# Kernel optimization log

Measured on AMD Instinct MI355X. Metric: run time of the kernel, lower is better.

The kernel has to match this reference:

```python
import jax, jax.numpy as jnp
import numpy as np

N_ENT = 100000
N_USR = 1024
E = 400000
D = 128
H = 4
R = 32


def setup_inputs() -> dict:
    key = jax.random.key(0)
    ks = jax.random.split(key, 9)
    a = float(np.sqrt(6.0 / (D + D)))  # xavier_uniform bound for [D, D]
    return {
        "entity_emb": jax.random.normal(ks[0], (N_ENT, D), dtype=jnp.float32),
        "user_emb": jax.random.normal(ks[1], (N_USR, D), dtype=jnp.float32),
        "interact_mat": jnp.zeros((1,), dtype=jnp.float32),  # unused by forward
        "weight": jax.random.normal(ks[2], (R, D), dtype=jnp.float32) * 0.1,
        "qTrans": jax.random.uniform(ks[3], (D, D), minval=-a, maxval=a, dtype=jnp.float32),
        "kTrans": jax.random.uniform(ks[4], (D, D), minval=-a, maxval=a, dtype=jnp.float32),
        "vTrans": jax.random.uniform(ks[5], (D, D), minval=-a, maxval=a, dtype=jnp.float32),
        "edge_index": jax.random.randint(ks[6], (2, E), 0, N_ENT, dtype=jnp.int64)
            if jax.config.jax_enable_x64 else jax.random.randint(ks[6], (2, E), 0, N_ENT, dtype=jnp.int32),
        "edge_type": jax.random.randint(ks[7], (E,), 1, R + 1, dtype=jnp.int32),  # types in [1, R]
        "layer": 0,
    }


def _kglayer(rows, col_embeds, embeds, n_seg, qT, kT, vT):
    # rows: [E] target-node index, col_embeds: [E, D] edge messages
    dh = D // H
    row_embeds = embeds[rows]                              # gather [E, D]
    q = (row_embeds @ qT).reshape(-1, H, dh)
    k = (col_embeds @ kT).reshape(-1, H, dh)
    v = (col_embeds @ vT).reshape(-1, H, dh)
    att = jnp.clip(jnp.einsum("ehd,ehd->eh", q, k), -10.0, 10.0)
    exp_att = jnp.exp(att)                                 # [E, H]
    att_norm = jax.ops.segment_sum(exp_att, rows, num_segments=n_seg)[rows]
    att = exp_att / (att_norm + 1e-8)
    res = (att[..., None] * v).reshape(-1, D)              # [E, D]
    return jax.ops.segment_sum(res, rows, num_segments=n_seg)


def _sim_hrt(head_emb, tail_emb, rel_emb):
    # per-edge scalar attention logit [E, 1]
    tr = jnp.linalg.norm(tail_emb * rel_emb, axis=1, keepdims=True)
    hr = jnp.linalg.norm(head_emb * rel_emb, axis=1, keepdims=True)
    return (hr * tr) ** 2


def reference(entity_emb, user_emb, interact_mat, weight, qTrans, kTrans, vTrans,
              edge_index, edge_type, layer):
    n_entities = entity_emb.shape[0]
    head, tail = edge_index[0], edge_index[1]
    rel = weight[edge_type - 1]                            # [E, D]
    neigh = entity_emb[tail] * rel                         # [E, D]
    kg_emb = _kglayer(head, neigh, entity_emb, n_entities, qTrans, kTrans, vTrans)
    w = _sim_hrt(kg_emb[head], kg_emb[tail], rel)          # [E, 1]
    w = jnp.broadcast_to(w, neigh.shape)                   # expand to [E, D]
    # scatter_softmax over edges sharing the same head (numerically stable)
    m = jax.ops.segment_max(w, head, num_segments=n_entities)[head]
    e = jnp.exp(w - m)
    s = jax.ops.segment_sum(e, head, num_segments=n_entities)[head]
    soft = e / s
    msg = soft * entity_emb[tail]
    return jax.ops.segment_sum(msg, head, num_segments=n_entities)
```

## Files before the change

kernel.cpp:

```cpp
#include <hip/hip_runtime.h>
#include <cstdint>

#define D 128
#define H 4
#define N_ENT 100000
#define N_EDGE 400000
#define R 32

#define SCAN_NB ((N_ENT + 511) / 512)

__global__ void k_hist(const int* __restrict__ head, int* __restrict__ deg) {
  const int e = blockIdx.x * 256 + threadIdx.x;
  if (e < N_EDGE) atomicAdd(&deg[head[e]], 1);
}

__global__ __launch_bounds__(256) void k_scan1(const int* __restrict__ deg,
                                               int* __restrict__ bsum) {
  const int t = threadIdx.x;
  const int i = blockIdx.x * 512 + t * 2;
  int v0 = (i < N_ENT) ? deg[i] : 0;
  int v1 = (i + 1 < N_ENT) ? deg[i + 1] : 0;
  int s = v0 + v1;
#pragma unroll
  for (int k = 1; k < 64; k <<= 1) s += __shfl_xor(s, k);
  __shared__ int ws[4];
  if ((t & 63) == 0) ws[t >> 6] = s;
  __syncthreads();
  if (t == 0) bsum[blockIdx.x] = ws[0] + ws[1] + ws[2] + ws[3];
}

__global__ __launch_bounds__(256) void k_scan2(const int* __restrict__ bsum,
                                               int* __restrict__ bbase,
                                               int* __restrict__ off) {
  __shared__ int sh[256];
  const int t = threadIdx.x;
  const int v = (t < SCAN_NB) ? bsum[t] : 0;
  sh[t] = v;
  __syncthreads();
  for (int d = 1; d < 256; d <<= 1) {
    const int u = (t >= d) ? sh[t - d] : 0;
    __syncthreads();
    sh[t] += u;
    __syncthreads();
  }
  if (t < SCAN_NB) bbase[t] = sh[t] - v;
  if (t == SCAN_NB - 1) off[N_ENT] = sh[t];
}

__global__ __launch_bounds__(256) void k_scan3(const int* __restrict__ deg,
                                               const int* __restrict__ bbase,
                                               int* __restrict__ off,
                                               int* __restrict__ cur) {
  __shared__ int sh[256];
  const int t = threadIdx.x;
  const int i = blockIdx.x * 512 + t * 2;
  const int v0 = (i < N_ENT) ? deg[i] : 0;
  const int v1 = (i + 1 < N_ENT) ? deg[i + 1] : 0;
  const int s = v0 + v1;
  sh[t] = s;
  __syncthreads();
  for (int d = 1; d < 256; d <<= 1) {
    const int u = (t >= d) ? sh[t - d] : 0;
    __syncthreads();
    sh[t] += u;
    __syncthreads();
  }
  const int ex = sh[t] - s + bbase[blockIdx.x];
  if (i < N_ENT) {
    off[i] = ex;
    cur[i] = ex;
  }
  if (i + 1 < N_ENT) {
    off[i + 1] = ex + v0;
    cur[i + 1] = ex + v0;
  }
}

__global__ void k_scatter(const int* __restrict__ head,
                          const int* __restrict__ tail,
                          const int* __restrict__ etype, int* __restrict__ cur,
                          int2* __restrict__ teP) {
  const int e = blockIdx.x * 256 + threadIdx.x;
  if (e >= N_EDGE) return;
  const int hd = head[e];
  const int pos = atomicAdd(&cur[hd], 1);
  teP[pos] = make_int2(tail[e], etype[e] - 1);
}

__global__ __launch_bounds__(256) void k_tr(const float* __restrict__ in,
                                            float* __restrict__ out) {
  __shared__ float tile[32][33];
  const int bx = blockIdx.x & 3, by = blockIdx.x >> 2;
  const int c = threadIdx.x & 31;
  const int r0 = (threadIdx.x >> 5) * 4;
#pragma unroll
  for (int i = 0; i < 4; ++i)
    tile[r0 + i][c] = in[(by * 32 + r0 + i) * 128 + bx * 32 + c];
  __syncthreads();
#pragma unroll
  for (int i = 0; i < 4; ++i)
    out[(bx * 32 + r0 + i) * 128 + by * 32 + c] = tile[c][r0 + i];
}

__global__ __launch_bounds__(512) void k_qproj(const float* __restrict__ ent,
                                               const float* __restrict__ qT,
                                               float* __restrict__ Q) {
  __shared__ float sT[D * D];
  __shared__ float rows[D * 128];
  const int t = threadIdx.x;
  const int n0 = blockIdx.x * 128;
#pragma unroll
  for (int s = 0; s < 8; ++s) {
    const int idx = (s * 512 + t) * 4;
    *(float4*)&sT[idx] = *(const float4*)&qT[idx];
  }
  {
    const int g = t & 3;
    const int n = t >> 2;
    const int node = n0 + n;
    if (node < N_ENT) {
      const float* src = ent + (size_t)node * D;
#pragma unroll
      for (int s = 0; s < 8; ++s) {
        const int i = s * 16 + g * 4;
        float4 v = *(const float4*)&src[i];
        rows[(i + 0) * 128 + n] = v.x;
        rows[(i + 1) * 128 + n] = v.y;
        rows[(i + 2) * 128 + n] = v.z;
        rows[(i + 3) * 128 + n] = v.w;
      }
    } else {
#pragma unroll
      for (int s = 0; s < 8; ++s) {
        const int i = s * 16 + g * 4;
        rows[(i + 0) * 128 + n] = 0.f;
        rows[(i + 1) * 128 + n] = 0.f;
        rows[(i + 2) * 128 + n] = 0.f;
        rows[(i + 3) * 128 + n] = 0.f;
      }
    }
  }
  __syncthreads();
  const int jj = t & 15;
  const int ee = t >> 4;
  float acc[4][8];
#pragma unroll
  for (int a = 0; a < 4; ++a)
#pragma unroll
    for (int b = 0; b < 8; ++b) acc[a][b] = 0.f;
#pragma unroll 4
  for (int i = 0; i < D; ++i) {
    float4 b0 = *(float4*)&sT[i * D + jj * 8];
    float4 b1 = *(float4*)&sT[i * D + jj * 8 + 4];
    float4 a0 = *(float4*)&rows[i * 128 + ee * 4];
    float bv[8] = {b0.x, b0.y, b0.z, b0.w, b1.x, b1.y, b1.z, b1.w};
    float av[4] = {a0.x, a0.y, a0.z, a0.w};
#pragma unroll
    for (int a = 0; a < 4; ++a)
#pragma unroll
      for (int b = 0; b < 8; ++b) acc[a][b] = fmaf(av[a], bv[b], acc[a][b]);
  }
#pragma unroll
  for (int a = 0; a < 4; ++a) {
    const int node = n0 + ee * 4 + a;
    if (node < N_ENT) {
      float4 o0 = {acc[a][0], acc[a][1], acc[a][2], acc[a][3]};
      float4 o1 = {acc[a][4], acc[a][5], acc[a][6], acc[a][7]};
      *(float4*)&Q[(size_t)node * D + jj * 8] = o0;
      *(float4*)&Q[(size_t)node * D + jj * 8 + 4] = o1;
    }
  }
}

__global__ __launch_bounds__(256, 8) void k_fused(
    const float* __restrict__ ent, const float* __restrict__ wrel,
    const float* __restrict__ kTt, const float* __restrict__ vT, float* qkg,
    const int* __restrict__ off, const int2* __restrict__ teP) {
  __shared__ float sQ[8 * 128];
  __shared__ float sPA[8 * 512];
  const int t = threadIdx.x;
  const int base = blockIdx.x * 8;

  const int wid = t >> 6;
  const int half = (t >> 5) & 1;
  const int l32 = t & 31;
  const int kk = wid * 2 + half;
  const int n = base + kk;

  {
    const int k = t >> 5;
    const int c4 = (t & 31) * 4;
    *(float4*)&sQ[k * 128 + c4] =
        *(const float4*)&qkg[(size_t)(base + k) * D + c4];
  }

  const int eb = off[n];
  const int deg = off[n + 1] - eb;
  float4 xv = {0, 0, 0, 0}, rv = {0, 0, 0, 0};
  if (deg > 0) {
    const int2 pf = teP[eb];
    xv = *(const float4*)&ent[(size_t)pf.x * D + l32 * 4];
    rv = *(const float4*)&wrel[(size_t)pf.y * D + l32 * 4];
  }
  __syncthreads();

  {
    const int i = t & 127;
    const int sub = t >> 7;
    float pp[2][8];
#pragma unroll
    for (int hh = 0; hh < 2; ++hh)
#pragma unroll
      for (int k = 0; k < 8; ++k) pp[hh][k] = 0.f;
#pragma unroll
    for (int hh = 0; hh < 2; ++hh) {
      const int h = sub * 2 + hh;
#pragma unroll 2
      for (int c4 = 0; c4 < 8; ++c4) {
        const float kv0 = kTt[(h * 32 + c4 * 4 + 0) * 128 + i];
        const float kv1 = kTt[(h * 32 + c4 * 4 + 1) * 128 + i];
        const float kv2 = kTt[(h * 32 + c4 * 4 + 2) * 128 + i];
        const float kv3 = kTt[(h * 32 + c4 * 4 + 3) * 128 + i];
#pragma unroll
        for (int k = 0; k < 8; ++k) {
          const float4 q = *(const float4*)&sQ[k * 128 + h * 32 + c4 * 4];
          pp[hh][k] = fmaf(kv0, q.x, pp[hh][k]);
          pp[hh][k] = fmaf(kv1, q.y, pp[hh][k]);
          pp[hh][k] = fmaf(kv2, q.z, pp[hh][k]);
          pp[hh][k] = fmaf(kv3, q.w, pp[hh][k]);
        }
      }
    }
#pragma unroll
    for (int hh = 0; hh < 2; ++hh)
#pragma unroll
      for (int k = 0; k < 8; ++k)
        sPA[k * 512 + (sub * 2 + hh) * 128 + i] = pp[hh][k];
  }
  __syncthreads();

  {
    const int lp = l32 & 3;
    const float4 P0 = *(const float4*)&sPA[kk * 512 + 0 * 128 + l32 * 4];
    const float4 P1 = *(const float4*)&sPA[kk * 512 + 1 * 128 + l32 * 4];
    const float4 P2 = *(const float4*)&sPA[kk * 512 + 2 * 128 + l32 * 4];
    const float4 P3 = *(const float4*)&sPA[kk * 512 + 3 * 128 + l32 * 4];
    float4 b0 = {0, 0, 0, 0}, b1 = {0, 0, 0, 0};
    float4 b2 = {0, 0, 0, 0}, b3 = {0, 0, 0, 0};
    float s0 = 0.f, s1 = 0.f, s2 = 0.f, s3 = 0.f;
    for (int idx = 0; idx < deg; ++idx) {
      const float4 cx = xv, cr = rv;
      if (idx + 1 < deg) {
        const int2 pf = teP[eb + idx + 1];
        xv = *(const float4*)&ent[(size_t)pf.x * D + l32 * 4];
        rv = *(const float4*)&wrel[(size_t)pf.y * D + l32 * 4];
      }
      const float4 nh = {cx.x * cr.x, cx.y * cr.y, cx.z * cr.z, cx.w * cr.w};
      float d0 = nh.x * P0.x + nh.y * P0.y + nh.z * P0.z + nh.w * P0.w;
      float d1 = nh.x * P1.x + nh.y * P1.y + nh.z * P1.z + nh.w * P1.w;
      float d2 = nh.x * P2.x + nh.y * P2.y + nh.z * P2.z + nh.w * P2.w;
      float d3 = nh.x * P3.x + nh.y * P3.y + nh.z * P3.z + nh.w * P3.w;
      float x01 = (l32 & 1) ? d1 : d0;
      float y01 = (l32 & 1) ? d0 : d1;
      x01 += __shfl_xor(y01, 1);
      float x23 = (l32 & 1) ? d3 : d2;
      float y23 = (l32 & 1) ? d2 : d3;
      x23 += __shfl_xor(y23, 1);
      float xa = (l32 & 2) ? x23 : x01;
      float xb = (l32 & 2) ? x01 : x23;
      xa += __shfl_xor(xb, 2);
      xa += __shfl_xor(xa, 4);
      xa += __shfl_xor(xa, 8);
      xa += __shfl_xor(xa, 16);
      const float eL = __expf(fminf(fmaxf(xa, -10.f), 10.f));
      const float e0 = eL;
      const float e1 = __shfl_xor(eL, 1);
      const float e2 = __shfl_xor(eL, 2);
      const float e3 = __shfl_xor(eL, 3);
      b0.x = fmaf(e0, nh.x, b0.x); b0.y = fmaf(e0, nh.y, b0.y);
      b0.z = fmaf(e0, nh.z, b0.z); b0.w = fmaf(e0, nh.w, b0.w);
      b1.x = fmaf(e1, nh.x, b1.x); b1.y = fmaf(e1, nh.y, b1.y);
      b1.z = fmaf(e1, nh.z, b1.z); b1.w = fmaf(e1, nh.w, b1.w);
      b2.x = fmaf(e2, nh.x, b2.x); b2.y = fmaf(e2, nh.y, b2.y);
      b2.z = fmaf(e2, nh.z, b2.z); b2.w = fmaf(e2, nh.w, b2.w);
      b3.x = fmaf(e3, nh.x, b3.x); b3.y = fmaf(e3, nh.y, b3.y);
      b3.z = fmaf(e3, nh.z, b3.z); b3.w = fmaf(e3, nh.w, b3.w);
      s0 += e0; s1 += e1; s2 += e2; s3 += e3;
    }
    const float i0 = 1.f / (s0 + 1e-8f);
    const float i1 = 1.f / (s1 + 1e-8f);
    const float i2 = 1.f / (s2 + 1e-8f);
    const float i3 = 1.f / (s3 + 1e-8f);
    float4 o0 = {b0.x * i0, b0.y * i0, b0.z * i0, b0.w * i0};
    float4 o1 = {b1.x * i1, b1.y * i1, b1.z * i1, b1.w * i1};
    float4 o2 = {b2.x * i2, b2.y * i2, b2.z * i2, b2.w * i2};
    float4 o3 = {b3.x * i3, b3.y * i3, b3.z * i3, b3.w * i3};
    const int sb = kk * 512 + l32 * 4;
    *(float4*)&sPA[sb + ((lp ^ 0) << 7)] = o0;
    *(float4*)&sPA[sb + ((lp ^ 1) << 7)] = o1;
    *(float4*)&sPA[sb + ((lp ^ 2) << 7)] = o2;
    *(float4*)&sPA[sb + ((lp ^ 3) << 7)] = o3;
  }
  __syncthreads();

  {
    const int c = t & 127;
    const int g4 = (t >> 7) * 4;
    const int h = c >> 5;
    float acc0 = 0.f, acc1 = 0.f, acc2 = 0.f, acc3 = 0.f;
    const float* agg0 = &sPA[(g4 + 0) * 512 + h * 128];
    const float* agg1 = &sPA[(g4 + 1) * 512 + h * 128];
    const float* agg2 = &sPA[(g4 + 2) * 512 + h * 128];
    const float* agg3 = &sPA[(g4 + 3) * 512 + h * 128];
#pragma unroll 4
    for (int d4 = 0; d4 < 32; ++d4) {
      const float4 a0 = *(const float4*)&agg0[d4 * 4];
      const float4 a1 = *(const float4*)&agg1[d4 * 4];
      const float4 a2 = *(const float4*)&agg2[d4 * 4];
      const float4 a3 = *(const float4*)&agg3[d4 * 4];
      const float v0 = vT[(d4 * 4 + 0) * 128 + c];
      const float v1 = vT[(d4 * 4 + 1) * 128 + c];
      const float v2 = vT[(d4 * 4 + 2) * 128 + c];
      const float v3 = vT[(d4 * 4 + 3) * 128 + c];
      acc0 = fmaf(a0.x, v0, acc0); acc0 = fmaf(a0.y, v1, acc0);
      acc0 = fmaf(a0.z, v2, acc0); acc0 = fmaf(a0.w, v3, acc0);
      acc1 = fmaf(a1.x, v0, acc1); acc1 = fmaf(a1.y, v1, acc1);
      acc1 = fmaf(a1.z, v2, acc1); acc1 = fmaf(a1.w, v3, acc1);
      acc2 = fmaf(a2.x, v0, acc2); acc2 = fmaf(a2.y, v1, acc2);
      acc2 = fmaf(a2.z, v2, acc2); acc2 = fmaf(a2.w, v3, acc2);
      acc3 = fmaf(a3.x, v0, acc3); acc3 = fmaf(a3.y, v1, acc3);
      acc3 = fmaf(a3.z, v2, acc3); acc3 = fmaf(a3.w, v3, acc3);
    }
    qkg[(size_t)(base + g4 + 0) * D + c] = acc0;
    qkg[(size_t)(base + g4 + 1) * D + c] = acc1;
    qkg[(size_t)(base + g4 + 2) * D + c] = acc2;
    qkg[(size_t)(base + g4 + 3) * D + c] = acc3;
  }
}

__global__ __launch_bounds__(256) void k_S(const float* __restrict__ kg,
                                           const float* __restrict__ wrel,
                                           float* __restrict__ S) {
  __shared__ float sB[D * 32];
  __shared__ float sA[D * 64];
  const int t = threadIdx.x;
  const int n0 = blockIdx.x * 64;
  {
    const int r = t & 31;
    const int qg = t >> 5;
#pragma unroll
    for (int s = 0; s < 4; ++s) {
      const int d = qg * 16 + s * 4;
      float4 b = *(const float4*)&wrel[(size_t)r * D + d];
      sB[(d + 0) * 32 + r] = b.x * b.x;
      sB[(d + 1) * 32 + r] = b.y * b.y;
      sB[(d + 2) * 32 + r] = b.z * b.z;
      sB[(d + 3) * 32 + r] = b.w * b.w;
    }
  }
  {
    const int nn = t & 63;
    const int dg = t >> 6;
    const int node = n0 + nn;
#pragma unroll
    for (int s = 0; s < 8; ++s) {
      const int d = dg * 32 + s * 4;
      float4 a = {0, 0, 0, 0};
      if (node < N_ENT) a = *(const float4*)&kg[(size_t)node * D + d];
      sA[(d + 0) * 64 + nn] = a.x * a.x;
      sA[(d + 1) * 64 + nn] = a.y * a.y;
      sA[(d + 2) * 64 + nn] = a.z * a.z;
      sA[(d + 3) * 64 + nn] = a.w * a.w;
    }
  }
  __syncthreads();
  const int nn2 = t >> 2;
  const int rg = t & 3;
  float acc[8];
#pragma unroll
  for (int c = 0; c < 8; ++c) acc[c] = 0.f;
#pragma unroll 4
  for (int d = 0; d < D; ++d) {
    const float a = sA[d * 64 + nn2];
    float4 b0 = *(float4*)&sB[d * 32 + rg * 8];
    float4 b1 = *(float4*)&sB[d * 32 + rg * 8 + 4];
    acc[0] = fmaf(a, b0.x, acc[0]);
    acc[1] = fmaf(a, b0.y, acc[1]);
    acc[2] = fmaf(a, b0.z, acc[2]);
    acc[3] = fmaf(a, b0.w, acc[3]);
    acc[4] = fmaf(a, b1.x, acc[4]);
    acc[5] = fmaf(a, b1.y, acc[5]);
    acc[6] = fmaf(a, b1.z, acc[6]);
    acc[7] = fmaf(a, b1.w, acc[7]);
  }
  const int node = n0 + nn2;
  if (node < N_ENT) {
    float4 o0 = {acc[0], acc[1], acc[2], acc[3]};
    float4 o1 = {acc[4], acc[5], acc[6], acc[7]};
    *(float4*)&S[(size_t)node * 32 + rg * 8] = o0;
    *(float4*)&S[(size_t)node * 32 + rg * 8 + 4] = o1;
  }
}

__global__ __launch_bounds__(256) void k_out2(
    const float* __restrict__ ent, const float* __restrict__ S,
    const int* __restrict__ off, const int2* __restrict__ teP,
    float* __restrict__ out) {
  const int t = threadIdx.x;
  const int wid = t >> 6;
  const int half = (t >> 5) & 1;
  const int l32 = t & 31;
  const int kk = wid * 2 + half;
  const int n = blockIdx.x * 8 + kk;
  if (n >= N_ENT) return;
  const int eb = off[n];
  const int deg = off[n + 1] - eb;
  const float sn = S[(size_t)n * 32 + l32];
  float4 acc = {0, 0, 0, 0};
  float m = 0.f, ssum = 0.f;
  for (int b = 0; b < deg; b += 32) {
    const int idx = b + l32;
    const bool val = idx < deg;
    const int e = eb + (val ? idx : 0);
    const int2 tp = teP[e];
    const int tl = tp.x;
    const int ty = tp.y;
    const float snv = __shfl(sn, ty, 32);
    float w = val ? snv * S[(size_t)tl * 32 + ty] : -1.f;
    float cm = w;
#pragma unroll
    for (int k = 1; k < 32; k <<= 1) cm = fmaxf(cm, __shfl_xor(cm, k));
    const float mnew = fmaxf(m, cm);
    const float scale = __expf(m - mnew);
    const float el = val ? __expf(w - mnew) : 0.f;
    float cs = el;
#pragma unroll
    for (int k = 1; k < 32; k <<= 1) cs += __shfl_xor(cs, k);
    ssum = ssum * scale + cs;
    acc.x *= scale; acc.y *= scale; acc.z *= scale; acc.w *= scale;
    const int cnt = (deg - b < 32) ? deg - b : 32;
    for (int j0 = 0; j0 < cnt; j0 += 4) {
      const int rem = cnt - j0;
      const int t0 = __shfl(tl, j0 + 0, 32);
      float4 r0 = *(const float4*)&ent[(size_t)t0 * D + l32 * 4];
      float4 r1, r2, r3;
      if (rem > 1) {
        const int t1 = __shfl(tl, j0 + 1, 32);
        r1 = *(const float4*)&ent[(size_t)t1 * D + l32 * 4];
      }
      if (rem > 2) {
        const int t2 = __shfl(tl, j0 + 2, 32);
        r2 = *(const float4*)&ent[(size_t)t2 * D + l32 * 4];
      }
      if (rem > 3) {
        const int t3 = __shfl(tl, j0 + 3, 32);
        r3 = *(const float4*)&ent[(size_t)t3 * D + l32 * 4];
      }
      const float w0 = __shfl(el, j0 + 0, 32);
      acc.x = fmaf(w0, r0.x, acc.x); acc.y = fmaf(w0, r0.y, acc.y);
      acc.z = fmaf(w0, r0.z, acc.z); acc.w = fmaf(w0, r0.w, acc.w);
      if (rem > 1) {
        const float w1 = __shfl(el, j0 + 1, 32);
        acc.x = fmaf(w1, r1.x, acc.x); acc.y = fmaf(w1, r1.y, acc.y);
        acc.z = fmaf(w1, r1.z, acc.z); acc.w = fmaf(w1, r1.w, acc.w);
      }
      if (rem > 2) {
        const float w2 = __shfl(el, j0 + 2, 32);
        acc.x = fmaf(w2, r2.x, acc.x); acc.y = fmaf(w2, r2.y, acc.y);
        acc.z = fmaf(w2, r2.z, acc.z); acc.w = fmaf(w2, r2.w, acc.w);
      }
      if (rem > 3) {
        const float w3 = __shfl(el, j0 + 3, 32);
        acc.x = fmaf(w3, r3.x, acc.x); acc.y = fmaf(w3, r3.y, acc.y);
        acc.z = fmaf(w3, r3.z, acc.z); acc.w = fmaf(w3, r3.w, acc.w);
      }
    }
    m = mnew;
  }
  const float inv = (deg > 0) ? 1.f / ssum : 0.f;
  float4 o = {acc.x * inv, acc.y * inv, acc.z * inv, acc.w * inv};
  *(float4*)&out[(size_t)n * D + l32 * 4] = o;
}

extern "C" void kernel_launch(void* const* d_in, const int* in_sizes, int n_in,
                              void* d_out, int out_size, void* d_ws,
                              size_t ws_size, hipStream_t stream) {
  const float* ent = (const float*)d_in[0];
  const float* wrel = (const float*)d_in[3];
  const float* qT = (const float*)d_in[4];
  const float* kT = (const float*)d_in[5];
  const float* vT = (const float*)d_in[6];
  const int* eidx = (const int*)d_in[7];
  const int* etype = (const int*)d_in[8];
  const int* head = eidx;
  const int* tail = eidx + N_EDGE;

  float* S = (float*)d_ws;
  int* off = (int*)(S + (size_t)N_ENT * 32);
  int* cur = off + (N_ENT + 2);
  int* deg = cur + N_ENT;
  int* bsum = deg + N_ENT;
  int* bbase = bsum + SCAN_NB;
  int2* teP = (int2*)(bbase + SCAN_NB);
  float* kTt = (float*)(teP + N_EDGE);
  float* qkg = (float*)d_out;

  hipMemsetAsync(deg, 0, N_ENT * sizeof(int), stream);
  k_hist<<<(N_EDGE + 255) / 256, 256, 0, stream>>>(head, deg);
  k_scan1<<<SCAN_NB, 256, 0, stream>>>(deg, bsum);
  k_scan2<<<1, 256, 0, stream>>>(bsum, bbase, off);
  k_scan3<<<SCAN_NB, 256, 0, stream>>>(deg, bbase, off, cur);
  k_scatter<<<(N_EDGE + 255) / 256, 256, 0, stream>>>(head, tail, etype, cur,
                                                      teP);
  k_tr<<<16, 256, 0, stream>>>(kT, kTt);
  k_qproj<<<(N_ENT + 127) / 128, 512, 0, stream>>>(ent, qT, qkg);
  k_fused<<<N_ENT / 8, 256, 0, stream>>>(ent, wrel, kTt, vT, qkg, off, teP);
  k_S<<<(N_ENT + 63) / 64, 256, 0, stream>>>(qkg, wrel, S);
  k_out2<<<(N_ENT + 7) / 8, 256, 0, stream>>>(ent, S, off, teP, qkg);
}
```

Measured before the change: 504.1 us.

## Sort nodes by degree via counting-sort permutation for load-balanced node processing

Adds a degree histogram, scan and scatter that build a permutation of nodes grouped by in-degree (capped at 63). The fused attention kernel and the output kernel then process nodes in that order, so nodes sharing a block or wavefront have similar edge counts and lanes diverge less. The cost is three extra small kernels plus a memset, one indirection per node, and scattered rather than contiguous row reads and writes of qkg. Buffers already used for the scan (cur, bsum, bbase) are reused for the permutation and bins.

```diff
diff --git a/kernel.cpp b/kernel.cpp
--- a/kernel.cpp
+++ b/kernel.cpp
@@ -87,6 +87,57 @@
   teP[pos] = make_int2(tail[e], etype[e] - 1);
 }
 
+__global__ __launch_bounds__(256) void k_dhist(const int* __restrict__ deg,
+                                               int* __restrict__ gbins) {
+  __shared__ int lb[64];
+  const int t = threadIdx.x;
+  if (t < 64) lb[t] = 0;
+  __syncthreads();
+  const int i = blockIdx.x * 256 + t;
+  if (i < N_ENT) {
+    int b = deg[i];
+    b = b > 63 ? 63 : b;
+    atomicAdd(&lb[b], 1);
+  }
+  __syncthreads();
+  if (t < 64 && lb[t] > 0) atomicAdd(&gbins[t], lb[t]);
+}
+
+__global__ void k_dscan(const int* __restrict__ gbins,
+                        int* __restrict__ gbase) {
+  const int t = threadIdx.x;
+  const int v = gbins[t];
+  int s = v;
+#pragma unroll
+  for (int k = 1; k < 64; k <<= 1) {
+    const int u = __shfl_up(s, k);
+    if (t >= k) s += u;
+  }
+  gbase[t] = s - v;
+}
+
+__global__ __launch_bounds__(256) void k_dscatter(const int* __restrict__ deg,
+                                                  int* __restrict__ gbase,
+                                                  int* __restrict__ perm) {
+  __shared__ int lb[64];
+  __shared__ int lstart[64];
+  const int t = threadIdx.x;
+  if (t < 64) lb[t] = 0;
+  __syncthreads();
+  const int i = blockIdx.x * 256 + t;
+  int b = 0, pos = 0;
+  const bool valid = i < N_ENT;
+  if (valid) {
+    b = deg[i];
+    b = b > 63 ? 63 : b;
+    pos = atomicAdd(&lb[b], 1);
+  }
+  __syncthreads();
+  if (t < 64) lstart[t] = (lb[t] > 0) ? atomicAdd(&gbase[t], lb[t]) : 0;
+  __syncthreads();
+  if (valid) perm[lstart[b] + pos] = i;
+}
+
 __global__ __launch_bounds__(256) void k_tr(const float* __restrict__ in,
                                             float* __restrict__ out) {
   __shared__ float tile[32][33];
@@ -175,7 +226,8 @@
 __global__ __launch_bounds__(256, 8) void k_fused(
     const float* __restrict__ ent, const float* __restrict__ wrel,
     const float* __restrict__ kTt, const float* __restrict__ vT, float* qkg,
-    const int* __restrict__ off, const int2* __restrict__ teP) {
+    const int* __restrict__ off, const int2* __restrict__ teP,
+    const int* __restrict__ perm) {
   __shared__ float sQ[8 * 128];
   __shared__ float sPA[8 * 512];
   const int t = threadIdx.x;
@@ -185,13 +237,14 @@
   const int half = (t >> 5) & 1;
   const int l32 = t & 31;
   const int kk = wid * 2 + half;
-  const int n = base + kk;
+  const int n = perm[base + kk];
 
   {
     const int k = t >> 5;
     const int c4 = (t & 31) * 4;
+    const int node = perm[base + k];
     *(float4*)&sQ[k * 128 + c4] =
-        *(const float4*)&qkg[(size_t)(base + k) * D + c4];
+        *(const float4*)&qkg[(size_t)node * D + c4];
   }
 
   const int eb = off[n];
@@ -331,10 +384,14 @@
       acc3 = fmaf(a3.x, v0, acc3); acc3 = fmaf(a3.y, v1, acc3);
       acc3 = fmaf(a3.z, v2, acc3); acc3 = fmaf(a3.w, v3, acc3);
     }
-    qkg[(size_t)(base + g4 + 0) * D + c] = acc0;
-    qkg[(size_t)(base + g4 + 1) * D + c] = acc1;
-    qkg[(size_t)(base + g4 + 2) * D + c] = acc2;
-    qkg[(size_t)(base + g4 + 3) * D + c] = acc3;
+    const int p0 = perm[base + g4 + 0];
+    const int p1 = perm[base + g4 + 1];
+    const int p2 = perm[base + g4 + 2];
+    const int p3 = perm[base + g4 + 3];
+    qkg[(size_t)p0 * D + c] = acc0;
+    qkg[(size_t)p1 * D + c] = acc1;
+    qkg[(size_t)p2 * D + c] = acc2;
+    qkg[(size_t)p3 * D + c] = acc3;
   }
 }
 
@@ -405,14 +462,15 @@
 __global__ __launch_bounds__(256) void k_out2(
     const float* __restrict__ ent, const float* __restrict__ S,
     const int* __restrict__ off, const int2* __restrict__ teP,
-    float* __restrict__ out) {
+    float* __restrict__ out, const int* __restrict__ perm) {
   const int t = threadIdx.x;
   const int wid = t >> 6;
   const int half = (t >> 5) & 1;
   const int l32 = t & 31;
   const int kk = wid * 2 + half;
-  const int n = blockIdx.x * 8 + kk;
-  if (n >= N_ENT) return;
+  const int slot = blockIdx.x * 8 + kk;
+  if (slot >= N_ENT) return;
+  const int n = perm[slot];
   const int eb = off[n];
   const int deg = off[n + 1] - eb;
   const float sn = S[(size_t)n * 32 + l32];
@@ -503,6 +561,9 @@
   int* bbase = bsum + SCAN_NB;
   int2* teP = (int2*)(bbase + SCAN_NB);
   float* kTt = (float*)(teP + N_EDGE);
+  int* perm = cur;
+  int* gbins = bsum;
+  int* gbase = bbase;
   float* qkg = (float*)d_out;
 
   hipMemsetAsync(deg, 0, N_ENT * sizeof(int), stream);
@@ -512,9 +573,14 @@
   k_scan3<<<SCAN_NB, 256, 0, stream>>>(deg, bbase, off, cur);
   k_scatter<<<(N_EDGE + 255) / 256, 256, 0, stream>>>(head, tail, etype, cur,
                                                       teP);
+  hipMemsetAsync(gbins, 0, 64 * sizeof(int), stream);
+  k_dhist<<<(N_ENT + 255) / 256, 256, 0, stream>>>(deg, gbins);
+  k_dscan<<<1, 64, 0, stream>>>(gbins, gbase);
+  k_dscatter<<<(N_ENT + 255) / 256, 256, 0, stream>>>(deg, gbase, perm);
   k_tr<<<16, 256, 0, stream>>>(kT, kTt);
   k_qproj<<<(N_ENT + 127) / 128, 512, 0, stream>>>(ent, qT, qkg);
-  k_fused<<<N_ENT / 8, 256, 0, stream>>>(ent, wrel, kTt, vT, qkg, off, teP);
+  k_fused<<<N_ENT / 8, 256, 0, stream>>>(ent, wrel, kTt, vT, qkg, off, teP,
+                                         perm);
   k_S<<<(N_ENT + 63) / 64, 256, 0, stream>>>(qkg, wrel, S);
-  k_out2<<<(N_ENT + 7) / 8, 256, 0, stream>>>(ent, S, off, teP, qkg);
-}
+  k_out2<<<(N_ENT + 7) / 8, 256, 0, stream>>>(ent, S, off, teP, qkg, perm);
+}
```

Measured after the change: 526.3 us. 4.4% more time.
